# Kernel tuning notes

Measured on AMD Instinct MI355X. Metric: run time of the kernel, lower is better.

Reference implementation:

```python
import jax, jax.numpy as jnp
import numpy as np

H = 16          # num_attention_heads
HD = 64         # attention_head_size
ALPHA = 1.5
BANDWIDTH = 1.0
A_EXP = 0.5     # sinkhorn-like exponent 'a'
DIST_SCALE = float(HD)  # alpha < 2 => scale by head_size
EPS = 1e-12     # F.normalize eps


def setup_inputs() -> dict:
    key = jax.random.key(0)
    ks = jax.random.split(key, 5)
    B, L, D = 2, 1024, 1024
    w_scale = 0.02  # keep distances in a non-degenerate range for the power-law kernel
    x = jax.random.normal(ks[0], (B, L, D), dtype=jnp.float32)
    WQ = jax.random.normal(ks[1], (D, D), dtype=jnp.float32) * w_scale
    WK = jax.random.normal(ks[2], (D, D), dtype=jnp.float32) * w_scale
    WV = jax.random.normal(ks[3], (D, D), dtype=jnp.float32) * w_scale
    WO = jax.random.normal(ks[4], (D, D), dtype=jnp.float32) * w_scale
    z = jnp.zeros((D,), dtype=jnp.float32)
    return {"x": x, "WQ": WQ, "bQ": z, "WK": WK, "bK": z,
            "WV": WV, "bV": z, "WO": WO, "bO": z}


def _heads(t, B, L):
    # [B, L, H*HD] -> [B, H, L, HD]
    return t.reshape(B, L, H, HD).transpose(0, 2, 1, 3)


def reference(x, WQ, bQ, WK, bK, WV, bV, WO, bO):
    B, L, D = x.shape
    q = _heads(x @ WQ + bQ, B, L)   # [B,H,L,HD]
    k = _heads(x @ WK + bK, B, L)
    v = _heads(x @ WV + bV, B, L)

    # torch.cdist(q, k, p=2): pairwise euclidean distance [B,H,L,L]
    q2 = jnp.sum(q * q, axis=-1)                      # [B,H,L]
    k2 = jnp.sum(k * k, axis=-1)                      # [B,H,L]
    qk = jnp.einsum('bhid,bhjd->bhij', q, k)          # [B,H,L,L]
    d2 = q2[..., :, None] + k2[..., None, :] - 2.0 * qk
    g_dist = jnp.sqrt(jnp.maximum(d2, EPS)) / DIST_SCALE

    # alpha < 2: power-law kernel (1 + g/sqrt(bw))^(-(d_intrinsic + alpha))
    attn_score = (1.0 + g_dist / np.sqrt(BANDWIDTH)) ** (-(HD + ALPHA))

    # a > 0: Sinkhorn-style row/col renormalization
    N_R = jnp.sum(attn_score, axis=-1)                # [B,H,L] row sums
    N_C = jnp.sum(attn_score, axis=-2)                # [B,H,L] col sums
    K_tilde = (N_R ** (-A_EXP))[..., :, None] * attn_score * (N_C ** (-A_EXP))[..., None, :]

    # F.normalize(p=1, dim=3); entries are positive so |.| sum == sum
    attention_probs = K_tilde / jnp.maximum(jnp.sum(K_tilde, axis=-1, keepdims=True), EPS)

    out = jnp.einsum('bhij,bhjd->bhid', attention_probs, v)   # [B,H,L,HD]
    out = out.transpose(0, 2, 1, 3).reshape(B, L, H * HD)
    return out @ WO + bO
```

## Files before the change

kernel.cpp:

```cpp
#include <hip/hip_runtime.h>
#include <math.h>


typedef __attribute__((ext_vector_type(8))) short short8;
typedef __attribute__((ext_vector_type(4))) float f32x4;

__device__ inline unsigned short f2bf(float f) {
  unsigned int u = __float_as_uint(f);
  unsigned int r = (u + 0x7FFFu + ((u >> 16) & 1u)) >> 16;
  return (unsigned short)r;
}
__device__ inline float bf2f(unsigned short s) {
  return __uint_as_float(((unsigned int)s) << 16);
}
__device__ inline float score_fn(float dot, float sq) {
  float d2 = fmaxf(fmaf(-2.f, dot, sq), 1e-12f);
  float sd = __builtin_amdgcn_sqrtf(d2);
  float lg = __builtin_amdgcn_logf(fmaf(sd, 0.015625f, 1.0f));
  return __builtin_amdgcn_exp2f(-65.5f * lg);
}
__device__ inline unsigned int cvtpk(float lo, float hi) {
  unsigned int r;
  asm("v_cvt_pk_bf16_f32 %0, %1, %2" : "=v"(r) : "v"(lo), "v"(hi));
  return r;
}
#define GLD16(lptr, gptr)                                                      \
  __builtin_amdgcn_global_load_lds(                                            \
      (const __attribute__((address_space(1))) void*)(gptr),                   \
      (__attribute__((address_space(3))) void*)(lptr), 16, 0, 0)

__global__ __launch_bounds__(256) void prep(const float* __restrict__ x,
                                            unsigned short* __restrict__ xb,
                                            const float* __restrict__ W0,
                                            const float* __restrict__ W1,
                                            const float* __restrict__ W2,
                                            const float* __restrict__ W3,
                                            unsigned short* __restrict__ T0,
                                            unsigned short* __restrict__ T1,
                                            unsigned short* __restrict__ T2,
                                            unsigned short* __restrict__ T3) {
  __shared__ float T[32][33];
  int bx = blockIdx.x;
  if (bx < 2048) {
    int i = bx * 256 + threadIdx.x;
    float4 v = ((const float4*)x)[i];
    xb[4 * i + 0] = f2bf(v.x);
    xb[4 * i + 1] = f2bf(v.y);
    xb[4 * i + 2] = f2bf(v.z);
    xb[4 * i + 3] = f2bf(v.w);
    return;
  }
  int idx = bx - 2048;
  int z = idx >> 10, rem = idx & 1023;
  const float* W = z == 0 ? W0 : z == 1 ? W1 : z == 2 ? W2 : W3;
  unsigned short* WT = z == 0 ? T0 : z == 1 ? T1 : z == 2 ? T2 : T3;
  int k0 = (rem >> 5) * 32, n0 = (rem & 31) * 32;
  int c = threadIdx.x & 31, r8 = threadIdx.x >> 5;
#pragma unroll
  for (int it = 0; it < 4; ++it) {
    int rr = r8 + it * 8;
    T[rr][c] = W[(size_t)(k0 + rr) * 1024 + n0 + c];
  }
  __syncthreads();
#pragma unroll
  for (int it = 0; it < 4; ++it) {
    int rr = r8 + it * 8;
    WT[(size_t)(n0 + rr) * 1024 + k0 + c] = f2bf(T[c][rr]);
  }
}

__global__ __launch_bounds__(512, 2) void gemm128k64(const unsigned short* __restrict__ A,
                                                     const unsigned short* __restrict__ B0,
                                                     const unsigned short* __restrict__ B1,
                                                     const unsigned short* __restrict__ B2,
                                                     const float* __restrict__ c0,
                                                     const float* __restrict__ c1,
                                                     const float* __restrict__ c2,
                                                     void* __restrict__ Y0,
                                                     void* __restrict__ Y1,
                                                     void* __restrict__ Y2,
                                                     float* __restrict__ sq0,
                                                     float* __restrict__ sq1,
                                                     float* __restrict__ sq2,
                                                     int m0, int m1, int m2) {
  int z = blockIdx.z;
  const unsigned short* BT = z == 0 ? B0 : z == 1 ? B1 : B2;
  const float* bias = z == 0 ? c0 : z == 1 ? c1 : c2;
  void* Y = z == 0 ? Y0 : z == 1 ? Y1 : Y2;
  float* sq = z == 0 ? sq0 : z == 1 ? sq1 : sq2;
  int mode = z == 0 ? m0 : z == 1 ? m1 : m2;

  __shared__ __align__(16) unsigned short As[2][128 * 64];
  __shared__ __align__(16) unsigned short Bs[2][128 * 64];
  int tid = threadIdx.x;
  int w = tid >> 6, l = tid & 63, g = l >> 4, l15 = l & 15;
  int wm = w >> 2, wn = w & 3;
  int bm = blockIdx.x * 128, bn = blockIdx.y * 128;
  const int x7 = l15 & 7;

  const int i0 = tid, i1 = tid + 512;
  const int r0 = i0 >> 3, s0 = (i0 & 7) ^ (r0 & 7);
  const int r1 = i1 >> 3, s1 = (i1 & 7) ^ (r1 & 7);

  GLD16(&As[0][i0 * 8], &A[(size_t)(bm + r0) * 1024 + s0 * 8]);
  GLD16(&As[0][i1 * 8], &A[(size_t)(bm + r1) * 1024 + s1 * 8]);
  GLD16(&Bs[0][i0 * 8], &BT[(size_t)(bn + r0) * 1024 + s0 * 8]);
  GLD16(&Bs[0][i1 * 8], &BT[(size_t)(bn + r1) * 1024 + s1 * 8]);

  f32x4 acc[4][2];
#pragma unroll
  for (int mi = 0; mi < 4; ++mi)
#pragma unroll
    for (int ni = 0; ni < 2; ++ni)
#pragma unroll
      for (int r = 0; r < 4; ++r) acc[mi][ni][r] = 0.f;

  __syncthreads();
  for (int t = 0; t < 16; ++t) {
    int cur = t & 1;
    if (t < 15) {
      int kn = (t + 1) * 64;
      GLD16(&As[cur ^ 1][i0 * 8], &A[(size_t)(bm + r0) * 1024 + kn + s0 * 8]);
      GLD16(&As[cur ^ 1][i1 * 8], &A[(size_t)(bm + r1) * 1024 + kn + s1 * 8]);
      GLD16(&Bs[cur ^ 1][i0 * 8], &BT[(size_t)(bn + r0) * 1024 + kn + s0 * 8]);
      GLD16(&Bs[cur ^ 1][i1 * 8], &BT[(size_t)(bn + r1) * 1024 + kn + s1 * 8]);
    }
#pragma unroll
    for (int kc = 0; kc < 2; ++kc) {
      const int cread = (((kc << 2) + g) ^ x7) * 8;
      short8 a[4], b[2];
#pragma unroll
      for (int mi = 0; mi < 4; ++mi)
        a[mi] = *(const short8*)&As[cur][(wm * 64 + mi * 16 + l15) * 64 + cread];
#pragma unroll
      for (int ni = 0; ni < 2; ++ni)
        b[ni] = *(const short8*)&Bs[cur][(wn * 32 + ni * 16 + l15) * 64 + cread];
#pragma unroll
      for (int mi = 0; mi < 4; ++mi)
#pragma unroll
        for (int ni = 0; ni < 2; ++ni)
          acc[mi][ni] = __builtin_amdgcn_mfma_f32_16x16x32_bf16(a[mi], b[ni], acc[mi][ni], 0, 0, 0);
    }
    __syncthreads();
  }

  float rowsq[4][4];
#pragma unroll
  for (int mi = 0; mi < 4; ++mi)
#pragma unroll
    for (int r = 0; r < 4; ++r) rowsq[mi][r] = 0.f;

#pragma unroll
  for (int ni = 0; ni < 2; ++ni) {
    int n = bn + wn * 32 + ni * 16 + l15;
    float bv = bias[n];
#pragma unroll
    for (int mi = 0; mi < 4; ++mi) {
#pragma unroll
      for (int r = 0; r < 4; ++r) {
        int m = bm + wm * 64 + mi * 16 + 4 * g + r;
        float v = acc[mi][ni][r] + bv;
        if (mode == 0) {
          int b = m >> 10, ll = m & 1023, h = n >> 6, hd = n & 63;
          unsigned short ush = f2bf(v);
          ((unsigned short*)Y)[(((size_t)(b * 16 + h) * 1024) + ll) * 64 + hd] = ush;
          float f = bf2f(ush);
          rowsq[mi][r] = fmaf(f, f, rowsq[mi][r]);
        } else if (mode == 1) {
          int b = m >> 10, ll = m & 1023, h = n >> 6, hd = n & 63;
          int jp = (ll & ~31) | (((ll >> 2) & 3) * 8 + ((ll >> 4) & 1) * 4 + (ll & 3));
          ((unsigned short*)Y)[(((size_t)(b * 16 + h) * 64) + hd) * 1024 + jp] = f2bf(v);
        } else {
          ((float*)Y)[(size_t)m * 1024 + n] = v;
        }
      }
    }
  }

  if (sq != nullptr) {
    float* Sq = (float*)&As[0][0];
#pragma unroll
    for (int mi = 0; mi < 4; ++mi)
#pragma unroll
      for (int r = 0; r < 4; ++r) {
        float s = rowsq[mi][r];
        s += __shfl_xor(s, 1);
        s += __shfl_xor(s, 2);
        s += __shfl_xor(s, 4);
        s += __shfl_xor(s, 8);
        rowsq[mi][r] = s;
      }
    if (l15 == 0) {
#pragma unroll
      for (int mi = 0; mi < 4; ++mi)
#pragma unroll
        for (int r = 0; r < 4; ++r)
          Sq[(wm * 4 + wn) * 64 + mi * 16 + 4 * g + r] = rowsq[mi][r];
    }
    __syncthreads();
    if (tid < 256) {
      int rr = tid & 127, hh = tid >> 7;
      float s = Sq[((rr >> 6) * 4 + 2 * hh) * 64 + (rr & 63)] +
                Sq[((rr >> 6) * 4 + 2 * hh + 1) * 64 + (rr & 63)];
      int m = bm + rr, b = m >> 10, ll = m & 1023;
      int h = (bn >> 6) + hh;
      sq[(size_t)(b * 16 + h) * 1024 + ll] = s;
    }
  }
}

__global__ __launch_bounds__(256) void gemm_st(const unsigned short* __restrict__ A,
                                               const unsigned short* __restrict__ BT,
                                               const float* __restrict__ bias,
                                               float* __restrict__ Y) {
  __shared__ __align__(16) unsigned short As[2][64 * 64];
  __shared__ __align__(16) unsigned short Bs[2][64 * 64];
  int tid = threadIdx.x;
  int w = tid >> 6, l = tid & 63, g = l >> 4, l15 = l & 15;
  int bm = blockIdx.x * 64, bn = blockIdx.y * 64;
  const int arow = w * 16 + l15;
  const int x7 = l15 & 7;

  const int i0s = tid, i1s = 256 + tid;
  const int r0 = i0s >> 3, s0 = (i0s & 7) ^ (r0 & 7);
  const int r1 = i1s >> 3, s1 = (i1s & 7) ^ (r1 & 7);

  GLD16(&As[0][i0s * 8], &A[(size_t)(bm + r0) * 1024 + s0 * 8]);
  GLD16(&As[0][i1s * 8], &A[(size_t)(bm + r1) * 1024 + s1 * 8]);
  GLD16(&Bs[0][i0s * 8], &BT[(size_t)(bn + r0) * 1024 + s0 * 8]);
  GLD16(&Bs[0][i1s * 8], &BT[(size_t)(bn + r1) * 1024 + s1 * 8]);

  f32x4 acc[4];
#pragma unroll
  for (int t = 0; t < 4; ++t)
#pragma unroll
    for (int r = 0; r < 4; ++r) acc[t][r] = 0.f;

  __syncthreads();
  for (int t = 0; t < 16; ++t) {
    int cur = t & 1;
    if (t < 15) {
      int kn = (t + 1) * 64;
      GLD16(&As[cur ^ 1][i0s * 8], &A[(size_t)(bm + r0) * 1024 + kn + s0 * 8]);
      GLD16(&As[cur ^ 1][i1s * 8], &A[(size_t)(bm + r1) * 1024 + kn + s1 * 8]);
      GLD16(&Bs[cur ^ 1][i0s * 8], &BT[(size_t)(bn + r0) * 1024 + kn + s0 * 8]);
      GLD16(&Bs[cur ^ 1][i1s * 8], &BT[(size_t)(bn + r1) * 1024 + kn + s1 * 8]);
    }
#pragma unroll
    for (int kc = 0; kc < 2; ++kc) {
      short8 a = *(const short8*)&As[cur][arow * 64 + ((kc * 4 + g) ^ x7) * 8];
#pragma unroll
      for (int tt = 0; tt < 4; ++tt) {
        short8 b = *(const short8*)&Bs[cur][(tt * 16 + l15) * 64 + ((kc * 4 + g) ^ x7) * 8];
        acc[tt] = __builtin_amdgcn_mfma_f32_16x16x32_bf16(a, b, acc[tt], 0, 0, 0);
      }
    }
    __syncthreads();
  }

#pragma unroll
  for (int t = 0; t < 4; ++t) {
    int n = bn + 16 * t + l15;
    float bv = bias[n];
#pragma unroll
    for (int r = 0; r < 4; ++r) {
      int m = bm + w * 16 + 4 * g + r;
      Y[(size_t)m * 1024 + n] = acc[t][r] + bv;
    }
  }
}

__global__ __launch_bounds__(256, 2) void colsum_mfma(const unsigned short* __restrict__ Qb,
                                                      const unsigned short* __restrict__ Kb,
                                                      const float* __restrict__ q2,
                                                      const float* __restrict__ k2,
                                                      float* __restrict__ rnc) {
  __shared__ __align__(16) unsigned short Qd[2][128 * 64];
  __shared__ __align__(16) float q2s[1024];
  int bh = blockIdx.x, jt = blockIdx.y;
  int tid = threadIdx.x, w = tid >> 6, l = tid & 63;
  int g = l >> 4, l15 = l & 15;
  const int x7 = l15 & 7;
  const unsigned short* Qp = Qb + (size_t)bh * 65536;
  const unsigned short* Kp = Kb + (size_t)bh * 65536;
  int j = jt * 64 + w * 16 + l15;

  int rQ[4], sQ[4];
#pragma unroll
  for (int it = 0; it < 4; ++it) {
    int c = tid + 256 * it;
    rQ[it] = c >> 3;
    sQ[it] = (c & 7) ^ (rQ[it] & 7);
  }

  GLD16(&q2s[tid * 4], q2 + (size_t)bh * 1024 + tid * 4);
#pragma unroll
  for (int it = 0; it < 4; ++it)
    GLD16(&Qd[0][(tid + 256 * it) * 8], Qp + (size_t)rQ[it] * 64 + sQ[it] * 8);

  short8 bk0 = *(const short8*)&Kp[(size_t)j * 64 + 8 * g];
  short8 bk1 = *(const short8*)&Kp[(size_t)j * 64 + 32 + 8 * g];
  float k2j = k2[(size_t)bh * 1024 + j];
  float colacc = 0.f;

  __syncthreads();
  for (int t = 0; t < 8; ++t) {
    int cur = t & 1;
    if (t < 7) {
      int inx = (t + 1) * 128;
#pragma unroll
      for (int it = 0; it < 4; ++it)
        GLD16(&Qd[cur ^ 1][(tid + 256 * it) * 8], Qp + (size_t)(inx + rQ[it]) * 64 + sQ[it] * 8);
    }
    const unsigned short* Ql = Qd[cur];
#pragma unroll
    for (int tp = 0; tp < 8; ++tp) {
      int rowb = (16 * tp + l15) * 64;
      short8 a0 = *(const short8*)&Ql[rowb + ((g) ^ x7) * 8];
      short8 a1 = *(const short8*)&Ql[rowb + ((4 + g) ^ x7) * 8];
      f32x4 cf;
#pragma unroll
      for (int r = 0; r < 4; ++r) cf[r] = 0.f;
      __builtin_amdgcn_s_setprio(1);
      cf = __builtin_amdgcn_mfma_f32_16x16x32_bf16(a0, bk0, cf, 0, 0, 0);
      cf = __builtin_amdgcn_mfma_f32_16x16x32_bf16(a1, bk1, cf, 0, 0, 0);
      __builtin_amdgcn_s_setprio(0);
      float4 qv = *(const float4*)&q2s[t * 128 + 16 * tp + 4 * g];
      colacc += score_fn(cf[0], qv.x + k2j);
      colacc += score_fn(cf[1], qv.y + k2j);
      colacc += score_fn(cf[2], qv.z + k2j);
      colacc += score_fn(cf[3], qv.w + k2j);
    }
    __syncthreads();
  }
  colacc += __shfl_xor(colacc, 16);
  colacc += __shfl_xor(colacc, 32);
  if (l < 16) rnc[(size_t)bh * 1024 + jt * 64 + w * 16 + l] = __builtin_amdgcn_rsqf(colacc);
}

__global__ __launch_bounds__(256, 2) void attn_mfma(const unsigned short* __restrict__ Qb,
                                                    const unsigned short* __restrict__ Kb,
                                                    const unsigned short* __restrict__ VTp,
                                                    const float* __restrict__ q2,
                                                    const float* __restrict__ k2,
                                                    const float* __restrict__ rnc,
                                                    unsigned short* __restrict__ AO) {
  __shared__ __align__(16) unsigned short Kd[2][128 * 64];
  __shared__ __align__(16) unsigned short Vd[2][64 * 128];
  __shared__ __align__(16) float k2s[1024];
  __shared__ __align__(16) float rns[1024];
  int bh = blockIdx.x;
  int tid = threadIdx.x, w = tid >> 6, l = tid & 63;
  int g = l >> 4, l15 = l & 15;
  const int x7 = l15 & 7;
  int it0 = blockIdx.y * 64 + w * 16;
  const unsigned short* Qp = Qb + (size_t)bh * 65536;
  const unsigned short* Kp = Kb + (size_t)bh * 65536;
  const unsigned short* Vp = VTp + (size_t)bh * 65536;
  int b = bh >> 4, h = bh & 15;

  int rK[4], cK[4], rV[4], cV[4];
#pragma unroll
  for (int it = 0; it < 4; ++it) {
    int c = tid + 256 * it;
    rK[it] = c >> 3;
    cK[it] = ((c & 7) ^ (rK[it] & 7));
    rV[it] = c >> 4;
    int s = c & 15;
    cV[it] = (s & 8) | ((s & 7) ^ (rV[it] & 7));
  }

  GLD16(&k2s[tid * 4], k2 + (size_t)bh * 1024 + tid * 4);
  GLD16(&rns[tid * 4], rnc + (size_t)bh * 1024 + tid * 4);
#pragma unroll
  for (int it = 0; it < 4; ++it) {
    GLD16(&Kd[0][(tid + 256 * it) * 8], Kp + (size_t)rK[it] * 64 + cK[it] * 8);
    GLD16(&Vd[0][(tid + 256 * it) * 8], Vp + (size_t)rV[it] * 1024 + cV[it] * 8);
  }

  short8 bq0 = *(const short8*)&Qp[(size_t)(it0 + l15) * 64 + 8 * g];
  short8 bq1 = *(const short8*)&Qp[(size_t)(it0 + l15) * 64 + 32 + 8 * g];
  float q2l = q2[(size_t)bh * 1024 + it0 + l15];

  f32x4 o[4];
#pragma unroll
  for (int t = 0; t < 4; ++t)
#pragma unroll
    for (int r = 0; r < 4; ++r) o[t][r] = 0.f;
  float dacc = 0.f;

  __syncthreads();
  for (int t = 0; t < 8; ++t) {
    int cur = t & 1;
    if (t < 7) {
      int j0n = (t + 1) * 128;
#pragma unroll
      for (int it = 0; it < 4; ++it) {
        GLD16(&Kd[cur ^ 1][(tid + 256 * it) * 8], Kp + (size_t)(j0n + rK[it]) * 64 + cK[it] * 8);
        GLD16(&Vd[cur ^ 1][(tid + 256 * it) * 8], Vp + (size_t)rV[it] * 1024 + j0n + cV[it] * 8);
      }
    }
    const unsigned short* Kl = Kd[cur];
    const unsigned short* Vl = Vd[cur];
#pragma unroll
    for (int jj = 0; jj < 2; ++jj) {
      float sc[16];
#pragma unroll
      for (int tp = 0; tp < 4; ++tp) {
        int rowb = (jj * 64 + 16 * tp + l15) * 64;
        short8 a0 = *(const short8*)&Kl[rowb + ((g) ^ x7) * 8];
        short8 a1 = *(const short8*)&Kl[rowb + ((4 + g) ^ x7) * 8];
        f32x4 cf;
#pragma unroll
        for (int r = 0; r < 4; ++r) cf[r] = 0.f;
        __builtin_amdgcn_s_setprio(1);
        cf = __builtin_amdgcn_mfma_f32_16x16x32_bf16(a0, bq0, cf, 0, 0, 0);
        cf = __builtin_amdgcn_mfma_f32_16x16x32_bf16(a1, bq1, cf, 0, 0, 0);
        __builtin_amdgcn_s_setprio(0);
        int base = t * 128 + jj * 64 + 16 * tp + 4 * g;
        float4 kv = *(const float4*)&k2s[base];
        float4 rv = *(const float4*)&rns[base];
        sc[tp * 4 + 0] = score_fn(cf[0], q2l + kv.x) * rv.x;
        sc[tp * 4 + 1] = score_fn(cf[1], q2l + kv.y) * rv.y;
        sc[tp * 4 + 2] = score_fn(cf[2], q2l + kv.z) * rv.z;
        sc[tp * 4 + 3] = score_fn(cf[3], q2l + kv.w) * rv.w;
      }
#pragma unroll
      for (int i = 0; i < 16; ++i) dacc += sc[i];
      int pi0[4], pi1[4];
      pi0[0] = (int)cvtpk(sc[0], sc[1]);
      pi0[1] = (int)cvtpk(sc[2], sc[3]);
      pi0[2] = (int)cvtpk(sc[4], sc[5]);
      pi0[3] = (int)cvtpk(sc[6], sc[7]);
      pi1[0] = (int)cvtpk(sc[8], sc[9]);
      pi1[1] = (int)cvtpk(sc[10], sc[11]);
      pi1[2] = (int)cvtpk(sc[12], sc[13]);
      pi1[3] = (int)cvtpk(sc[14], sc[15]);
      short8 pa0 = *(short8*)pi0;
      short8 pa1 = *(short8*)pi1;
#pragma unroll
      for (int t5 = 0; t5 < 4; ++t5) {
        int vr = 16 * t5 + l15;
        short8 bv0 = *(const short8*)&Vl[vr * 128 + (jj * 8 + ((g) ^ x7)) * 8];
        short8 bv1 = *(const short8*)&Vl[vr * 128 + (jj * 8 + ((4 + g) ^ x7)) * 8];
        __builtin_amdgcn_s_setprio(1);
        o[t5] = __builtin_amdgcn_mfma_f32_16x16x32_bf16(pa0, bv0, o[t5], 0, 0, 0);
        o[t5] = __builtin_amdgcn_mfma_f32_16x16x32_bf16(pa1, bv1, o[t5], 0, 0, 0);
        __builtin_amdgcn_s_setprio(0);
      }
    }
    __syncthreads();
  }

  dacc += __shfl_xor(dacc, 16);
  dacc += __shfl_xor(dacc, 32);
  float dv[4];
#pragma unroll
  for (int r = 0; r < 4; ++r) dv[r] = __shfl(dacc, 4 * g + r);

#pragma unroll
  for (int t = 0; t < 4; ++t) {
#pragma unroll
    for (int r = 0; r < 4; ++r) {
      int m = b * 1024 + it0 + 4 * g + r;
      int n = h * 64 + t * 16 + l15;
      AO[(size_t)m * 1024 + n] = f2bf(o[t][r] / dv[r]);
    }
  }
}

extern "C" void kernel_launch(void* const* d_in, const int* in_sizes, int n_in,
                              void* d_out, int out_size, void* d_ws, size_t ws_size,
                              hipStream_t stream) {
  const float* x  = (const float*)d_in[0];
  const float* WQ = (const float*)d_in[1];
  const float* bQ = (const float*)d_in[2];
  const float* WK = (const float*)d_in[3];
  const float* bK = (const float*)d_in[4];
  const float* WV = (const float*)d_in[5];
  const float* bV = (const float*)d_in[6];
  const float* WO = (const float*)d_in[7];
  const float* bO = (const float*)d_in[8];

  char* base = (char*)d_ws;
  unsigned short* xb  = (unsigned short*)(base);
  unsigned short* WQT = (unsigned short*)(base + (4u  << 20));
  unsigned short* WKT = (unsigned short*)(base + (6u  << 20));
  unsigned short* WVT = (unsigned short*)(base + (8u  << 20));
  unsigned short* WOT = (unsigned short*)(base + (10u << 20));
  unsigned short* Qb  = (unsigned short*)(base + (12u << 20));
  unsigned short* Kb  = (unsigned short*)(base + (16u << 20));
  unsigned short* VTp = (unsigned short*)(base + (20u << 20));
  unsigned short* AOb = (unsigned short*)(base + (24u << 20));
  float* q2  = (float*)(base + (28u << 20));
  float* k2  = (float*)(base + (28u << 20) + (128u << 10));
  float* rnc = (float*)(base + (28u << 20) + (256u << 10));

  prep<<<6144, 256, 0, stream>>>(x, xb, WQ, WK, WV, WO, WQT, WKT, WVT, WOT);

  gemm128k64<<<dim3(16, 8, 3), 512, 0, stream>>>(xb, WQT, WKT, WVT, bQ, bK, bV,
                                                 Qb, Kb, VTp, q2, k2, nullptr,
                                                 0, 0, 1);

  colsum_mfma<<<dim3(32, 16), 256, 0, stream>>>(Qb, Kb, q2, k2, rnc);
  attn_mfma<<<dim3(32, 16), 256, 0, stream>>>(Qb, Kb, VTp, q2, k2, rnc, AOb);

  gemm_st<<<dim3(32, 16), 256, 0, stream>>>(AOb, WOT, bO, (float*)d_out);
}
```

Before: 98.72 us.

## Triple-buffer K/V/Q tiles with 64-row stages and explicit vmcnt waits

Both the colsum and attention kernels move from 128-row double buffers to 64-row triple buffers. Loads are issued two stages ahead, and each iteration ends with an explicit s_waitcnt on the vector-memory counter plus a raw s_barrier instead of __syncthreads, so prefetches stay in flight across iterations. colsum also raises its launch-bounds occupancy hint from 2 to 4 blocks per CU, and the smaller LDS footprint helps that. The risks are that the manual vmcnt accounting can be wrong given the other global loads in flight, and that halving the stage size doubles the number of barriers.

```diff
diff --git a/kernel.cpp b/kernel.cpp
--- a/kernel.cpp
+++ b/kernel.cpp
@@ -28,6 +28,12 @@
   __builtin_amdgcn_global_load_lds(                                            \
       (const __attribute__((address_space(1))) void*)(gptr),                   \
       (__attribute__((address_space(3))) void*)(lptr), 16, 0, 0)
+#define MEMFENCE() asm volatile("" ::: "memory")
+#define HARD_BARRIER()                 \
+  do {                                 \
+    __builtin_amdgcn_s_barrier();      \
+    MEMFENCE();                        \
+  } while (0)
 
 __global__ __launch_bounds__(256) void prep(const float* __restrict__ x,
                                             unsigned short* __restrict__ xb,
@@ -270,12 +276,12 @@
   }
 }
 
-__global__ __launch_bounds__(256, 2) void colsum_mfma(const unsigned short* __restrict__ Qb,
+__global__ __launch_bounds__(256, 4) void colsum_mfma(const unsigned short* __restrict__ Qb,
                                                       const unsigned short* __restrict__ Kb,
                                                       const float* __restrict__ q2,
                                                       const float* __restrict__ k2,
                                                       float* __restrict__ rnc) {
-  __shared__ __align__(16) unsigned short Qd[2][128 * 64];
+  __shared__ __align__(16) unsigned short Qd[3][64 * 64];
   __shared__ __align__(16) float q2s[1024];
   int bh = blockIdx.x, jt = blockIdx.y;
   int tid = threadIdx.x, w = tid >> 6, l = tid & 63;
@@ -285,36 +291,36 @@
   const unsigned short* Kp = Kb + (size_t)bh * 65536;
   int j = jt * 64 + w * 16 + l15;
 
-  int rQ[4], sQ[4];
-#pragma unroll
-  for (int it = 0; it < 4; ++it) {
-    int c = tid + 256 * it;
-    rQ[it] = c >> 3;
-    sQ[it] = (c & 7) ^ (rQ[it] & 7);
-  }
+  const int i0s = tid, i1s = 256 + tid;
+  const int r0 = i0s >> 3, s0 = (i0s & 7) ^ (r0 & 7);
+  const int r1 = i1s >> 3, s1 = (i1s & 7) ^ (r1 & 7);
 
   GLD16(&q2s[tid * 4], q2 + (size_t)bh * 1024 + tid * 4);
-#pragma unroll
-  for (int it = 0; it < 4; ++it)
-    GLD16(&Qd[0][(tid + 256 * it) * 8], Qp + (size_t)rQ[it] * 64 + sQ[it] * 8);
+  GLD16(&Qd[0][i0s * 8], Qp + (size_t)r0 * 64 + s0 * 8);
+  GLD16(&Qd[0][i1s * 8], Qp + (size_t)r1 * 64 + s1 * 8);
+  GLD16(&Qd[1][i0s * 8], Qp + (size_t)(64 + r0) * 64 + s0 * 8);
+  GLD16(&Qd[1][i1s * 8], Qp + (size_t)(64 + r1) * 64 + s1 * 8);
 
   short8 bk0 = *(const short8*)&Kp[(size_t)j * 64 + 8 * g];
   short8 bk1 = *(const short8*)&Kp[(size_t)j * 64 + 32 + 8 * g];
   float k2j = k2[(size_t)bh * 1024 + j];
   float colacc = 0.f;
 
-  __syncthreads();
-  for (int t = 0; t < 8; ++t) {
-    int cur = t & 1;
-    if (t < 7) {
-      int inx = (t + 1) * 128;
-#pragma unroll
-      for (int it = 0; it < 4; ++it)
-        GLD16(&Qd[cur ^ 1][(tid + 256 * it) * 8], Qp + (size_t)(inx + rQ[it]) * 64 + sQ[it] * 8);
-    }
-    const unsigned short* Ql = Qd[cur];
-#pragma unroll
-    for (int tp = 0; tp < 8; ++tp) {
+  asm volatile("s_waitcnt vmcnt(2)" ::: "memory");
+  HARD_BARRIER();
+
+  for (int t = 0; t < 16; ++t) {
+    int cur = t % 3;
+    if (t < 14) {
+      int nb = (t + 2) % 3;
+      int inx = (t + 2) * 64;
+      GLD16(&Qd[nb][i0s * 8], Qp + (size_t)(inx + r0) * 64 + s0 * 8);
+      GLD16(&Qd[nb][i1s * 8], Qp + (size_t)(inx + r1) * 64 + s1 * 8);
+    }
+    MEMFENCE();
+    const unsigned short* Ql = &Qd[cur][0];
+#pragma unroll
+    for (int tp = 0; tp < 4; ++tp) {
       int rowb = (16 * tp + l15) * 64;
       short8 a0 = *(const short8*)&Ql[rowb + ((g) ^ x7) * 8];
       short8 a1 = *(const short8*)&Ql[rowb + ((4 + g) ^ x7) * 8];
@@ -325,13 +331,18 @@
       cf = __builtin_amdgcn_mfma_f32_16x16x32_bf16(a0, bk0, cf, 0, 0, 0);
       cf = __builtin_amdgcn_mfma_f32_16x16x32_bf16(a1, bk1, cf, 0, 0, 0);
       __builtin_amdgcn_s_setprio(0);
-      float4 qv = *(const float4*)&q2s[t * 128 + 16 * tp + 4 * g];
+      float4 qv = *(const float4*)&q2s[t * 64 + 16 * tp + 4 * g];
       colacc += score_fn(cf[0], qv.x + k2j);
       colacc += score_fn(cf[1], qv.y + k2j);
       colacc += score_fn(cf[2], qv.z + k2j);
       colacc += score_fn(cf[3], qv.w + k2j);
     }
-    __syncthreads();
+    if (t < 14) {
+      asm volatile("s_waitcnt vmcnt(2)" ::: "memory");
+    } else {
+      asm volatile("s_waitcnt vmcnt(0)" ::: "memory");
+    }
+    HARD_BARRIER();
   }
   colacc += __shfl_xor(colacc, 16);
   colacc += __shfl_xor(colacc, 32);
@@ -345,8 +356,8 @@
                                                     const float* __restrict__ k2,
                                                     const float* __restrict__ rnc,
                                                     unsigned short* __restrict__ AO) {
-  __shared__ __align__(16) unsigned short Kd[2][128 * 64];
-  __shared__ __align__(16) unsigned short Vd[2][64 * 128];
+  __shared__ __align__(16) unsigned short Kd[3][64 * 64];
+  __shared__ __align__(16) unsigned short Vd[3][64 * 64];
   __shared__ __align__(16) float k2s[1024];
   __shared__ __align__(16) float rns[1024];
   int bh = blockIdx.x;
@@ -359,24 +370,20 @@
   const unsigned short* Vp = VTp + (size_t)bh * 65536;
   int b = bh >> 4, h = bh & 15;
 
-  int rK[4], cK[4], rV[4], cV[4];
-#pragma unroll
-  for (int it = 0; it < 4; ++it) {
-    int c = tid + 256 * it;
-    rK[it] = c >> 3;
-    cK[it] = ((c & 7) ^ (rK[it] & 7));
-    rV[it] = c >> 4;
-    int s = c & 15;
-    cV[it] = (s & 8) | ((s & 7) ^ (rV[it] & 7));
-  }
+  const int i0s = tid, i1s = 256 + tid;
+  const int r0 = i0s >> 3, s0 = (i0s & 7) ^ (r0 & 7);
+  const int r1 = i1s >> 3, s1 = (i1s & 7) ^ (r1 & 7);
 
   GLD16(&k2s[tid * 4], k2 + (size_t)bh * 1024 + tid * 4);
   GLD16(&rns[tid * 4], rnc + (size_t)bh * 1024 + tid * 4);
-#pragma unroll
-  for (int it = 0; it < 4; ++it) {
-    GLD16(&Kd[0][(tid + 256 * it) * 8], Kp + (size_t)rK[it] * 64 + cK[it] * 8);
-    GLD16(&Vd[0][(tid + 256 * it) * 8], Vp + (size_t)rV[it] * 1024 + cV[it] * 8);
-  }
+  GLD16(&Kd[0][i0s * 8], Kp + (size_t)r0 * 64 + s0 * 8);
+  GLD16(&Kd[0][i1s * 8], Kp + (size_t)r1 * 64 + s1 * 8);
+  GLD16(&Vd[0][i0s * 8], Vp + (size_t)r0 * 1024 + s0 * 8);
+  GLD16(&Vd[0][i1s * 8], Vp + (size_t)r1 * 1024 + s1 * 8);
+  GLD16(&Kd[1][i0s * 8], Kp + (size_t)(64 + r0) * 64 + s0 * 8);
+  GLD16(&Kd[1][i1s * 8], Kp + (size_t)(64 + r1) * 64 + s1 * 8);
+  GLD16(&Vd[1][i0s * 8], Vp + (size_t)r0 * 1024 + 64 + s0 * 8);
+  GLD16(&Vd[1][i1s * 8], Vp + (size_t)r1 * 1024 + 64 + s1 * 8);
 
   short8 bq0 = *(const short8*)&Qp[(size_t)(it0 + l15) * 64 + 8 * g];
   short8 bq1 = *(const short8*)&Qp[(size_t)(it0 + l15) * 64 + 32 + 8 * g];
@@ -389,67 +396,72 @@
     for (int r = 0; r < 4; ++r) o[t][r] = 0.f;
   float dacc = 0.f;
 
-  __syncthreads();
-  for (int t = 0; t < 8; ++t) {
-    int cur = t & 1;
-    if (t < 7) {
-      int j0n = (t + 1) * 128;
-#pragma unroll
-      for (int it = 0; it < 4; ++it) {
-        GLD16(&Kd[cur ^ 1][(tid + 256 * it) * 8], Kp + (size_t)(j0n + rK[it]) * 64 + cK[it] * 8);
-        GLD16(&Vd[cur ^ 1][(tid + 256 * it) * 8], Vp + (size_t)rV[it] * 1024 + j0n + cV[it] * 8);
-      }
-    }
-    const unsigned short* Kl = Kd[cur];
-    const unsigned short* Vl = Vd[cur];
-#pragma unroll
-    for (int jj = 0; jj < 2; ++jj) {
-      float sc[16];
-#pragma unroll
-      for (int tp = 0; tp < 4; ++tp) {
-        int rowb = (jj * 64 + 16 * tp + l15) * 64;
-        short8 a0 = *(const short8*)&Kl[rowb + ((g) ^ x7) * 8];
-        short8 a1 = *(const short8*)&Kl[rowb + ((4 + g) ^ x7) * 8];
-        f32x4 cf;
-#pragma unroll
-        for (int r = 0; r < 4; ++r) cf[r] = 0.f;
-        __builtin_amdgcn_s_setprio(1);
-        cf = __builtin_amdgcn_mfma_f32_16x16x32_bf16(a0, bq0, cf, 0, 0, 0);
-        cf = __builtin_amdgcn_mfma_f32_16x16x32_bf16(a1, bq1, cf, 0, 0, 0);
-        __builtin_amdgcn_s_setprio(0);
-        int base = t * 128 + jj * 64 + 16 * tp + 4 * g;
-        float4 kv = *(const float4*)&k2s[base];
-        float4 rv = *(const float4*)&rns[base];
-        sc[tp * 4 + 0] = score_fn(cf[0], q2l + kv.x) * rv.x;
-        sc[tp * 4 + 1] = score_fn(cf[1], q2l + kv.y) * rv.y;
-        sc[tp * 4 + 2] = score_fn(cf[2], q2l + kv.z) * rv.z;
-        sc[tp * 4 + 3] = score_fn(cf[3], q2l + kv.w) * rv.w;
-      }
-#pragma unroll
-      for (int i = 0; i < 16; ++i) dacc += sc[i];
-      int pi0[4], pi1[4];
-      pi0[0] = (int)cvtpk(sc[0], sc[1]);
-      pi0[1] = (int)cvtpk(sc[2], sc[3]);
-      pi0[2] = (int)cvtpk(sc[4], sc[5]);
-      pi0[3] = (int)cvtpk(sc[6], sc[7]);
-      pi1[0] = (int)cvtpk(sc[8], sc[9]);
-      pi1[1] = (int)cvtpk(sc[10], sc[11]);
-      pi1[2] = (int)cvtpk(sc[12], sc[13]);
-      pi1[3] = (int)cvtpk(sc[14], sc[15]);
-      short8 pa0 = *(short8*)pi0;
-      short8 pa1 = *(short8*)pi1;
-#pragma unroll
-      for (int t5 = 0; t5 < 4; ++t5) {
-        int vr = 16 * t5 + l15;
-        short8 bv0 = *(const short8*)&Vl[vr * 128 + (jj * 8 + ((g) ^ x7)) * 8];
-        short8 bv1 = *(const short8*)&Vl[vr * 128 + (jj * 8 + ((4 + g) ^ x7)) * 8];
-        __builtin_amdgcn_s_setprio(1);
-        o[t5] = __builtin_amdgcn_mfma_f32_16x16x32_bf16(pa0, bv0, o[t5], 0, 0, 0);
-        o[t5] = __builtin_amdgcn_mfma_f32_16x16x32_bf16(pa1, bv1, o[t5], 0, 0, 0);
-        __builtin_amdgcn_s_setprio(0);
-      }
-    }
-    __syncthreads();
+  asm volatile("s_waitcnt vmcnt(4)" ::: "memory");
+  HARD_BARRIER();
+
+  for (int t = 0; t < 16; ++t) {
+    int cur = t % 3;
+    if (t < 14) {
+      int nb = (t + 2) % 3;
+      int j0n = (t + 2) * 64;
+      GLD16(&Kd[nb][i0s * 8], Kp + (size_t)(j0n + r0) * 64 + s0 * 8);
+      GLD16(&Kd[nb][i1s * 8], Kp + (size_t)(j0n + r1) * 64 + s1 * 8);
+      GLD16(&Vd[nb][i0s * 8], Vp + (size_t)r0 * 1024 + j0n + s0 * 8);
+      GLD16(&Vd[nb][i1s * 8], Vp + (size_t)r1 * 1024 + j0n + s1 * 8);
+    }
+    MEMFENCE();
+    const unsigned short* Kl = &Kd[cur][0];
+    const unsigned short* Vl = &Vd[cur][0];
+    int j0 = t * 64;
+    float sc[16];
+#pragma unroll
+    for (int tp = 0; tp < 4; ++tp) {
+      int rowb = (16 * tp + l15) * 64;
+      short8 a0 = *(const short8*)&Kl[rowb + ((g) ^ x7) * 8];
+      short8 a1 = *(const short8*)&Kl[rowb + ((4 + g) ^ x7) * 8];
+      f32x4 cf;
+#pragma unroll
+      for (int r = 0; r < 4; ++r) cf[r] = 0.f;
+      __builtin_amdgcn_s_setprio(1);
+      cf = __builtin_amdgcn_mfma_f32_16x16x32_bf16(a0, bq0, cf, 0, 0, 0);
+      cf = __builtin_amdgcn_mfma_f32_16x16x32_bf16(a1, bq1, cf, 0, 0, 0);
+      __builtin_amdgcn_s_setprio(0);
+      float4 kv = *(const float4*)&k2s[j0 + 16 * tp + 4 * g];
+      float4 rv = *(const float4*)&rns[j0 + 16 * tp + 4 * g];
+      sc[tp * 4 + 0] = score_fn(cf[0], q2l + kv.x) * rv.x;
+      sc[tp * 4 + 1] = score_fn(cf[1], q2l + kv.y) * rv.y;
+      sc[tp * 4 + 2] = score_fn(cf[2], q2l + kv.z) * rv.z;
+      sc[tp * 4 + 3] = score_fn(cf[3], q2l + kv.w) * rv.w;
+    }
+#pragma unroll
+    for (int i = 0; i < 16; ++i) dacc += sc[i];
+    int pi0[4], pi1[4];
+    pi0[0] = (int)cvtpk(sc[0], sc[1]);
+    pi0[1] = (int)cvtpk(sc[2], sc[3]);
+    pi0[2] = (int)cvtpk(sc[4], sc[5]);
+    pi0[3] = (int)cvtpk(sc[6], sc[7]);
+    pi1[0] = (int)cvtpk(sc[8], sc[9]);
+    pi1[1] = (int)cvtpk(sc[10], sc[11]);
+    pi1[2] = (int)cvtpk(sc[12], sc[13]);
+    pi1[3] = (int)cvtpk(sc[14], sc[15]);
+    short8 pa0 = *(short8*)pi0;
+    short8 pa1 = *(short8*)pi1;
+#pragma unroll
+    for (int t5 = 0; t5 < 4; ++t5) {
+      int rowb = (16 * t5 + l15) * 64;
+      short8 v0 = *(const short8*)&Vl[rowb + ((g) ^ x7) * 8];
+      short8 v1 = *(const short8*)&Vl[rowb + ((4 + g) ^ x7) * 8];
+      __builtin_amdgcn_s_setprio(1);
+      o[t5] = __builtin_amdgcn_mfma_f32_16x16x32_bf16(pa0, v0, o[t5], 0, 0, 0);
+      o[t5] = __builtin_amdgcn_mfma_f32_16x16x32_bf16(pa1, v1, o[t5], 0, 0, 0);
+      __builtin_amdgcn_s_setprio(0);
+    }
+    if (t < 14) {
+      asm volatile("s_waitcnt vmcnt(4)" ::: "memory");
+    } else {
+      asm volatile("s_waitcnt vmcnt(0)" ::: "memory");
+    }
+    HARD_BARRIER();
   }
 
   dacc += __shfl_xor(dacc, 16);
```

Result: no change. 98.28 us (-0.4%).
